# Kernel optimization log

Hardware: AMD Instinct MI355X
Metric: run time of the kernel (lower is better)

## Reference

```python
import jax, jax.numpy as jnp
import numpy as np

MAX_DIST = 32
NUM_HEADS = 16


def setup_inputs() -> dict:
    key = jax.random.key(0)
    ks = jax.random.split(key, 10)
    D = 1024
    B, S = 2, 2048
    hd = D // NUM_HEADS
    sc = 0.02
    return {
        "x": jax.random.normal(ks[0], (B, S, D), dtype=jnp.float32),
        "Wq": jax.random.normal(ks[1], (D, D), dtype=jnp.float32) * sc,
        "bq": jax.random.normal(ks[2], (D,), dtype=jnp.float32) * sc,
        "Wk": jax.random.normal(ks[3], (D, D), dtype=jnp.float32) * sc,
        "bk": jax.random.normal(ks[4], (D,), dtype=jnp.float32) * sc,
        "Wv": jax.random.normal(ks[5], (D, D), dtype=jnp.float32) * sc,
        "bv": jax.random.normal(ks[6], (D,), dtype=jnp.float32) * sc,
        "Wo": jax.random.normal(ks[7], (D, D), dtype=jnp.float32) * sc,
        "bo": jax.random.normal(ks[8], (D,), dtype=jnp.float32) * sc,
        "rel_emb": jax.random.normal(ks[9], (2 * MAX_DIST + 1, hd), dtype=jnp.float32) * sc,
    }


def reference(x, Wq, bq, Wk, bk, Wv, bv, Wo, bo, rel_emb):
    B, S, D = x.shape
    H = NUM_HEADS
    hd = D // H
    scale = hd ** -0.5

    def proj(W, b):
        # [B,S,D] -> [B,H,S,hd]
        return (x @ W + b).reshape(B, S, H, hd).transpose(0, 2, 1, 3)

    q = proj(Wq, bq)
    k = proj(Wk, bk)
    v = proj(Wv, bv)

    # relative position embedding lookup: [S,S,hd]
    pos = jnp.arange(S)
    rel = jnp.clip(pos[:, None] - pos[None, :], -MAX_DIST, MAX_DIST) + MAX_DIST
    rpe = rel_emb[rel]  # [S,S,hd]

    cc = jnp.einsum('bhqd,bhkd->bhqk', q, k) * scale
    cp = jnp.einsum('bhqd,qkd->bhqk', q, rpe) * scale
    attn = jax.nn.softmax(cc + cp, axis=-1)
    ctx = jnp.einsum('bhqk,bhkd->bhqd', attn, v)  # [B,H,S,hd]
    ctx = ctx.transpose(0, 2, 1, 3).reshape(B, S, D)
    return ctx @ Wo + bo
```

## Files before the change

kernel.cpp:

```cpp
#include <hip/hip_runtime.h>

typedef __attribute__((ext_vector_type(4))) float f32x4;
typedef __attribute__((ext_vector_type(8))) short bf16x8;

#define SEQ    2048
#define HD     64
#define NBH    32
#define MTOK   4096
#define DMODEL 1024
#define QBLK   128

__device__ __forceinline__ unsigned short f2b(float f) {
  unsigned int u = __float_as_uint(f);
  u += 0x7fffu + ((u >> 16) & 1u);
  return (unsigned short)(u >> 16);
}
__device__ __forceinline__ float b2f(unsigned short s) {
  return __uint_as_float(((unsigned int)s) << 16);
}
__device__ __forceinline__ unsigned int cvtpk_bf16(float lo, float hi) {
  unsigned int r;
  asm("v_cvt_pk_bf16_f32 %0, %1, %2" : "=v"(r) : "v"(lo), "v"(hi));
  return r;
}
__device__ __forceinline__ void gload16(const void* g, void* l) {
  __builtin_amdgcn_global_load_lds(
      (const __attribute__((address_space(1))) unsigned int*)g,
      (__attribute__((address_space(3))) unsigned int*)l, 16, 0, 0);
}

__global__ __launch_bounds__(256) void k_convert_x(const float* __restrict__ x,
                                                   unsigned short* __restrict__ xb) {
  int i = blockIdx.x * 256 + threadIdx.x;
  float4 v = ((const float4*)x)[i];
  ushort4 o;
  o.x = f2b(v.x); o.y = f2b(v.y); o.z = f2b(v.z); o.w = f2b(v.w);
  ((ushort4*)xb)[i] = o;
}

__global__ __launch_bounds__(256) void k_wtrans_all(const float* __restrict__ Wq,
                                                    const float* __restrict__ Wk,
                                                    const float* __restrict__ Wv,
                                                    const float* __restrict__ Wo,
                                                    unsigned short* __restrict__ Wqkv,
                                                    unsigned short* __restrict__ Wot) {
  __shared__ float tile[64 * 65];
  int z = blockIdx.z;
  const float* W = (z == 0) ? Wq : (z == 1) ? Wk : (z == 2) ? Wv : Wo;
  unsigned short* Wt = (z == 3) ? Wot : Wqkv + (size_t)z * DMODEL * DMODEL;
  int bi = blockIdx.x, bj = blockIdx.y, t = threadIdx.x;
  for (int p = 0; p < 16; p++) {
    int e = p * 256 + t;
    int r = e >> 6, c = e & 63;
    tile[r * 65 + c] = W[(size_t)(bi * 64 + r) * DMODEL + bj * 64 + c];
  }
  __syncthreads();
  for (int p = 0; p < 16; p++) {
    int e = p * 256 + t;
    int n = e >> 6, k = e & 63;
    Wt[(size_t)(bj * 64 + n) * DMODEL + bi * 64 + k] = f2b(tile[k * 65 + n]);
  }
}

template <int MODE>
__global__ __launch_bounds__(256) void k_gemm_bt(
    const unsigned short* __restrict__ A, const unsigned short* __restrict__ Bt,
    int M, int N, int K,
    const float* __restrict__ bias0, const float* __restrict__ bias1,
    const float* __restrict__ bias2,
    float* __restrict__ Cf,
    unsigned short* __restrict__ Qo, unsigned short* __restrict__ Ko,
    unsigned short* __restrict__ Vo) {
  __shared__ unsigned short As[128 * 64];
  __shared__ unsigned short Bs[128 * 64];
  int bm = blockIdx.x, bn = blockIdx.y;
  int tid = threadIdx.x;
  int w = tid >> 6, lane = tid & 63;
  int lg = lane >> 4, lc = lane & 15;
  int wm = (w >> 1) * 64, wn = (w & 1) * 64;
  f32x4 acc[4][4];
  for (int a = 0; a < 4; a++)
    for (int b = 0; b < 4; b++) acc[a][b] = (f32x4){0.f, 0.f, 0.f, 0.f};
  const unsigned short* ag = A + (size_t)(bm * 128) * K;
  const unsigned short* bg = Bt + (size_t)(bn * 128) * K;
  for (int k0 = 0; k0 < K; k0 += 64) {
    __syncthreads();
    for (int p = 0; p < 4; p++) {
      int c = (w * 4 + p) * 64 + lane;
      int r = c >> 3, ch = (c & 7) ^ (r & 7);
      gload16(ag + (size_t)r * K + k0 + ch * 8, &As[c * 8]);
      gload16(bg + (size_t)r * K + k0 + ch * 8, &Bs[c * 8]);
    }
    __syncthreads();
    for (int kk = 0; kk < 2; kk++) {
      bf16x8 av[4], bv[4];
      for (int mi = 0; mi < 4; mi++) {
        int row = wm + mi * 16 + lc;
        av[mi] = *(const bf16x8*)&As[row * 64 + ((kk * 32 + lg * 8) ^ ((row & 7) << 3))];
      }
      for (int ni = 0; ni < 4; ni++) {
        int row = wn + ni * 16 + lc;
        bv[ni] = *(const bf16x8*)&Bs[row * 64 + ((kk * 32 + lg * 8) ^ ((row & 7) << 3))];
      }
      for (int mi = 0; mi < 4; mi++)
        for (int ni = 0; ni < 4; ni++)
          acc[mi][ni] = __builtin_amdgcn_mfma_f32_16x16x32_bf16(av[mi], bv[ni], acc[mi][ni], 0, 0, 0);
    }
  }
  for (int mi = 0; mi < 4; mi++) {
    for (int i = 0; i < 4; i++) {
      int row = bm * 128 + wm + mi * 16 + 4 * lg + i;
      for (int ni = 0; ni < 4; ni++) {
        int col = bn * 128 + wn + ni * 16 + lc;
        float v = acc[mi][ni][i];
        if (MODE == 0) {
          Cf[(size_t)row * N + col] = v + bias0[col];
        } else {
          int which = col >> 10, hcol = col & 1023;
          const float* bb = which == 0 ? bias0 : (which == 1 ? bias1 : bias2);
          unsigned short* dst = which == 0 ? Qo : (which == 1 ? Ko : Vo);
          int b = row >> 11, s = row & 2047;
          int h = hcol >> 6, d = hcol & 63;
          dst[(((size_t)(b * 16 + h)) * SEQ + s) * HD + d] = f2b(v + bb[hcol]);
        }
      }
    }
  }
}

__global__ __launch_bounds__(256) void k_tvqr(const unsigned short* __restrict__ V,
                                              unsigned short* __restrict__ Vt,
                                              const unsigned short* __restrict__ Qb,
                                              const float* __restrict__ rel_emb,
                                              unsigned short* __restrict__ qr) {
  __shared__ unsigned short tile[64 * 72];
  __shared__ float relS[65 * 66];
  __shared__ unsigned short qS[32 * 64];
  int bh = blockIdx.y, t = threadIdx.x;
  if (blockIdx.x < 32) {
    int s0 = blockIdx.x * 64;
    for (int p = 0; p < 16; p++) {
      int e = p * 256 + t;
      int r = e >> 6, c = e & 63;
      tile[r * 72 + c] = V[(((size_t)bh) * SEQ + s0 + r) * HD + c];
    }
    __syncthreads();
    for (int p = 0; p < 16; p++) {
      int e = p * 256 + t;
      int d = e >> 6, j = e & 63;
      Vt[(((size_t)bh) * HD + d) * SEQ + s0 + j] = tile[j * 72 + d];
    }
  } else {
    int s0 = (blockIdx.x - 32) * 32;
    for (int i = t; i < 65 * 64; i += 256) relS[(i >> 6) * 66 + (i & 63)] = rel_emb[i];
    for (int i = t; i < 32 * 64; i += 256) qS[i] = Qb[((size_t)bh * SEQ + s0) * HD + i];
    __syncthreads();
    for (int e = t; e < 32 * 65; e += 256) {
      int sl = e / 65, r = e % 65;
      float acc = 0.f;
      for (int d = 0; d < 64; d++) acc += b2f(qS[sl * 64 + d]) * relS[r * 66 + d];
      qr[((size_t)bh * SEQ + s0 + sl) * 65 + r] = f2b(acc);
    }
  }
}

#define C1 0.180336880f
#define C2 11.5415603f
__global__ __launch_bounds__(512, 4) void k_attn(const unsigned short* __restrict__ Qb,
                                                 const unsigned short* __restrict__ Kb,
                                                 const unsigned short* __restrict__ Vtb,
                                                 const unsigned short* __restrict__ qr,
                                                 unsigned short* __restrict__ ctx) {
  __shared__ unsigned short Ks[64 * 64];
  __shared__ unsigned short Vts[64 * 64];
  __shared__ unsigned short Ps[8][16 * 64];
  __shared__ unsigned short qrs[QBLK * 65];
  int bh = blockIdx.x, qt = blockIdx.y;
  int tid = threadIdx.x, w = tid >> 6, lane = tid & 63;
  int lg = lane >> 4, lc = lane & 15;
  int q0 = qt * QBLK, qw = q0 + w * 16;

  {
    const unsigned int* src = (const unsigned int*)(qr + ((size_t)bh * SEQ + q0) * 65);
    for (int i = tid; i < QBLK * 65 / 2; i += 512) ((unsigned int*)qrs)[i] = src[i];
  }
  bf16x8 aq[2];
  {
    const unsigned short* qp = Qb + ((size_t)bh * SEQ + qw + lc) * HD + lg * 8;
    aq[0] = *(const bf16x8*)qp;
    aq[1] = *(const bf16x8*)(qp + 32);
  }
  f32x4 o[4];
  float l[4];
  for (int n = 0; n < 4; n++) o[n] = (f32x4){0.f, 0.f, 0.f, 0.f};
  for (int i = 0; i < 4; i++) l[i] = 0.f;
  __syncthreads();

  float blo[4], bhi[4];
  for (int i = 0; i < 4; i++) {
    int rl = w * 16 + 4 * lg + i;
    blo[i] = fmaf(b2f(qrs[rl * 65]),      C1, -C2);
    bhi[i] = fmaf(b2f(qrs[rl * 65 + 64]), C1, -C2);
  }

  for (int kt = 0; kt < SEQ / 64; kt++) {
    int k0 = kt * 64;
    const unsigned short* kg = Kb + ((size_t)bh * SEQ + k0) * HD;
    const unsigned short* vg = Vtb + ((size_t)bh * HD) * SEQ + k0;
    {
      int c = tid;
      int r = c >> 3, ch = (c & 7) ^ (r & 7);
      gload16(kg + (size_t)r * HD + ch * 8, &Ks[c * 8]);
      gload16(vg + (size_t)r * SEQ + ch * 8, &Vts[c * 8]);
    }
    __syncthreads();

    f32x4 s[4];
    #pragma unroll
    for (int n = 0; n < 4; n++) s[n] = (f32x4){0.f, 0.f, 0.f, 0.f};
    __builtin_amdgcn_s_setprio(1);
    #pragma unroll
    for (int n = 0; n < 4; n++) {
      int row = n * 16 + lc;
      #pragma unroll
      for (int kk = 0; kk < 2; kk++) {
        bf16x8 bk = *(const bf16x8*)&Ks[row * 64 + ((kk * 32 + lg * 8) ^ ((row & 7) << 3))];
        s[n] = __builtin_amdgcn_mfma_f32_16x16x32_bf16(aq[kk], bk, s[n], 0, 0, 0);
      }
    }
    __builtin_amdgcn_s_setprio(0);

    int dw = qw - k0;
    bool gather = (dw >= -32) && (dw <= 80);
    #pragma unroll
    for (int n = 0; n < 4; n++)
      #pragma unroll
      for (int i = 0; i < 4; i++) {
        float bf;
        if (gather) {
          int rl = w * 16 + 4 * lg + i;
          int rel = rl + q0 - k0 - n * 16 - lc;
          rel = rel < -32 ? -32 : (rel > 32 ? 32 : rel);
          bf = fmaf(b2f(qrs[rl * 65 + rel + 32]), C1, -C2);
        } else {
          bf = (dw < 0) ? blo[i] : bhi[i];
        }
        float p = __builtin_amdgcn_exp2f(fmaf(s[n][i], C1, bf));
        s[n][i] = p;
        l[i] += p;
      }

    #pragma unroll
    for (int n = 0; n < 4; n++)
      #pragma unroll
      for (int i = 0; i < 4; i += 2) {
        unsigned int u = cvtpk_bf16(s[n][i], s[n][i + 1]);
        int r0 = 4 * lg + i, r1 = r0 + 1;
        Ps[w][r0 * 64 + ((n * 16 + lc) ^ ((r0 & 7) << 3))] = (unsigned short)u;
        Ps[w][r1 * 64 + ((n * 16 + lc) ^ ((r1 & 7) << 3))] = (unsigned short)(u >> 16);
      }

    __builtin_amdgcn_s_setprio(1);
    #pragma unroll
    for (int kk = 0; kk < 2; kk++) {
      bf16x8 ap = *(const bf16x8*)&Ps[w][lc * 64 + ((kk * 32 + lg * 8) ^ ((lc & 7) << 3))];
      #pragma unroll
      for (int n = 0; n < 4; n++) {
        int row = n * 16 + lc;
        bf16x8 bv = *(const bf16x8*)&Vts[row * 64 + ((kk * 32 + lg * 8) ^ ((row & 7) << 3))];
        o[n] = __builtin_amdgcn_mfma_f32_16x16x32_bf16(ap, bv, o[n], 0, 0, 0);
      }
    }
    __builtin_amdgcn_s_setprio(0);
    __syncthreads();
  }

  int b = bh >> 4, h = bh & 15;
  for (int i = 0; i < 4; i++) {
    float t = l[i];
    t += __shfl_xor(t, 1);
    t += __shfl_xor(t, 2);
    t += __shfl_xor(t, 4);
    t += __shfl_xor(t, 8);
    float inv = 1.f / t;
    int row = qw + 4 * lg + i;
    size_t base = ((size_t)(b * SEQ + row)) * DMODEL + h * HD;
    for (int n = 0; n < 4; n++) ctx[base + n * 16 + lc] = f2b(o[n][i] * inv);
  }
}

extern "C" void kernel_launch(void* const* d_in, const int* in_sizes, int n_in,
                              void* d_out, int out_size, void* d_ws, size_t ws_size,
                              hipStream_t stream) {
  const float* x   = (const float*)d_in[0];
  const float* Wq  = (const float*)d_in[1];
  const float* bq  = (const float*)d_in[2];
  const float* Wk  = (const float*)d_in[3];
  const float* bk  = (const float*)d_in[4];
  const float* Wv  = (const float*)d_in[5];
  const float* bv  = (const float*)d_in[6];
  const float* Wo  = (const float*)d_in[7];
  const float* bo  = (const float*)d_in[8];
  const float* rel = (const float*)d_in[9];
  float* out = (float*)d_out;

  char* ws = (char*)d_ws;
  size_t off = 0;
  auto carve = [&](size_t bytes) -> void* {
    void* p = ws + off;
    off += (bytes + 255) & ~(size_t)255;
    return p;
  };
  unsigned short* xb   = (unsigned short*)carve((size_t)MTOK * DMODEL * 2);
  unsigned short* Wqkv = (unsigned short*)carve((size_t)3 * DMODEL * DMODEL * 2);
  unsigned short* Wot  = (unsigned short*)carve((size_t)DMODEL * DMODEL * 2);
  unsigned short* Qb   = (unsigned short*)carve((size_t)NBH * SEQ * HD * 2);
  unsigned short* Kb   = (unsigned short*)carve((size_t)NBH * SEQ * HD * 2);
  unsigned short* Vb   = (unsigned short*)carve((size_t)NBH * SEQ * HD * 2);
  unsigned short* Vtb  = (unsigned short*)carve((size_t)NBH * SEQ * HD * 2);
  unsigned short* qr   = (unsigned short*)carve((size_t)NBH * SEQ * 65 * 2);
  unsigned short* ctx  = (unsigned short*)carve((size_t)MTOK * DMODEL * 2);

  k_convert_x<<<MTOK * DMODEL / 4 / 256, 256, 0, stream>>>(x, xb);
  k_wtrans_all<<<dim3(16, 16, 4), 256, 0, stream>>>(Wq, Wk, Wv, Wo, Wqkv, Wot);
  k_gemm_bt<1><<<dim3(32, 24), 256, 0, stream>>>(xb, Wqkv, MTOK, 3 * DMODEL, DMODEL,
                                                 bq, bk, bv, nullptr, Qb, Kb, Vb);
  k_tvqr<<<dim3(96, 32), 256, 0, stream>>>(Vb, Vtb, Qb, rel, qr);
  k_attn<<<dim3(NBH, SEQ / QBLK), 512, 0, stream>>>(Qb, Kb, Vtb, qr, ctx);
  k_gemm_bt<0><<<dim3(32, 8), 256, 0, stream>>>(ctx, Wot, MTOK, DMODEL, DMODEL,
                                                bo, nullptr, nullptr, out,
                                                nullptr, nullptr, nullptr);
}
```

Measured before the change: 174.9 us.

## Give each attention wave 32 query rows to reuse K/V fragments

```diff
diff --git a/kernel.cpp b/kernel.cpp
--- a/kernel.cpp
+++ b/kernel.cpp
@@ -166,58 +166,63 @@
 
 #define C1 0.180336880f
 #define C2 11.5415603f
-__global__ __launch_bounds__(512, 4) void k_attn(const unsigned short* __restrict__ Qb,
+__global__ __launch_bounds__(256, 3) void k_attn(const unsigned short* __restrict__ Qb,
                                                  const unsigned short* __restrict__ Kb,
                                                  const unsigned short* __restrict__ Vtb,
                                                  const unsigned short* __restrict__ qr,
                                                  unsigned short* __restrict__ ctx) {
   __shared__ unsigned short Ks[64 * 64];
   __shared__ unsigned short Vts[64 * 64];
-  __shared__ unsigned short Ps[8][16 * 64];
+  __shared__ unsigned short Ps[4][32 * 64];
   __shared__ unsigned short qrs[QBLK * 65];
   int bh = blockIdx.x, qt = blockIdx.y;
   int tid = threadIdx.x, w = tid >> 6, lane = tid & 63;
   int lg = lane >> 4, lc = lane & 15;
-  int q0 = qt * QBLK, qw = q0 + w * 16;
+  int q0 = qt * QBLK, qw = q0 + w * 32;
 
   {
     const unsigned int* src = (const unsigned int*)(qr + ((size_t)bh * SEQ + q0) * 65);
-    for (int i = tid; i < QBLK * 65 / 2; i += 512) ((unsigned int*)qrs)[i] = src[i];
-  }
-  bf16x8 aq[2];
-  {
-    const unsigned short* qp = Qb + ((size_t)bh * SEQ + qw + lc) * HD + lg * 8;
-    aq[0] = *(const bf16x8*)qp;
-    aq[1] = *(const bf16x8*)(qp + 32);
-  }
-  f32x4 o[4];
-  float l[4];
-  for (int n = 0; n < 4; n++) o[n] = (f32x4){0.f, 0.f, 0.f, 0.f};
-  for (int i = 0; i < 4; i++) l[i] = 0.f;
+    for (int i = tid; i < QBLK * 65 / 2; i += 256) ((unsigned int*)qrs)[i] = src[i];
+  }
+  bf16x8 aq[2][2];
+  for (int m = 0; m < 2; m++) {
+    const unsigned short* qp = Qb + ((size_t)bh * SEQ + qw + m * 16 + lc) * HD + lg * 8;
+    aq[m][0] = *(const bf16x8*)qp;
+    aq[m][1] = *(const bf16x8*)(qp + 32);
+  }
+  f32x4 o[2][4];
+  float l[2][4];
+  for (int m = 0; m < 2; m++)
+    for (int n = 0; n < 4; n++) o[m][n] = (f32x4){0.f, 0.f, 0.f, 0.f};
+  for (int m = 0; m < 2; m++)
+    for (int i = 0; i < 4; i++) l[m][i] = 0.f;
   __syncthreads();
 
-  float blo[4], bhi[4];
-  for (int i = 0; i < 4; i++) {
-    int rl = w * 16 + 4 * lg + i;
-    blo[i] = fmaf(b2f(qrs[rl * 65]),      C1, -C2);
-    bhi[i] = fmaf(b2f(qrs[rl * 65 + 64]), C1, -C2);
-  }
+  float blo[2][4], bhi[2][4];
+  for (int m = 0; m < 2; m++)
+    for (int i = 0; i < 4; i++) {
+      int rl = w * 32 + m * 16 + 4 * lg + i;
+      blo[m][i] = fmaf(b2f(qrs[rl * 65]),      C1, -C2);
+      bhi[m][i] = fmaf(b2f(qrs[rl * 65 + 64]), C1, -C2);
+    }
 
   for (int kt = 0; kt < SEQ / 64; kt++) {
     int k0 = kt * 64;
     const unsigned short* kg = Kb + ((size_t)bh * SEQ + k0) * HD;
     const unsigned short* vg = Vtb + ((size_t)bh * HD) * SEQ + k0;
-    {
-      int c = tid;
-      int r = c >> 3, ch = (c & 7) ^ (r & 7);
-      gload16(kg + (size_t)r * HD + ch * 8, &Ks[c * 8]);
-      gload16(vg + (size_t)r * SEQ + ch * 8, &Vts[c * 8]);
-    }
-    __syncthreads();
-
-    f32x4 s[4];
-    #pragma unroll
-    for (int n = 0; n < 4; n++) s[n] = (f32x4){0.f, 0.f, 0.f, 0.f};
+    #pragma unroll
+    for (int p = 0; p < 2; p++) {
+      int idx = p * 256 + tid;
+      int r = idx >> 3, ch = (idx & 7) ^ (r & 7);
+      gload16(kg + (size_t)r * HD + ch * 8, &Ks[idx * 8]);
+      gload16(vg + (size_t)r * SEQ + ch * 8, &Vts[idx * 8]);
+    }
+    __syncthreads();
+
+    f32x4 s[2][4];
+    #pragma unroll
+    for (int m = 0; m < 2; m++)
+      for (int n = 0; n < 4; n++) s[m][n] = (f32x4){0.f, 0.f, 0.f, 0.f};
     __builtin_amdgcn_s_setprio(1);
     #pragma unroll
     for (int n = 0; n < 4; n++) {
@@ -225,50 +230,59 @@
       #pragma unroll
       for (int kk = 0; kk < 2; kk++) {
         bf16x8 bk = *(const bf16x8*)&Ks[row * 64 + ((kk * 32 + lg * 8) ^ ((row & 7) << 3))];
-        s[n] = __builtin_amdgcn_mfma_f32_16x16x32_bf16(aq[kk], bk, s[n], 0, 0, 0);
+        s[0][n] = __builtin_amdgcn_mfma_f32_16x16x32_bf16(aq[0][kk], bk, s[0][n], 0, 0, 0);
+        s[1][n] = __builtin_amdgcn_mfma_f32_16x16x32_bf16(aq[1][kk], bk, s[1][n], 0, 0, 0);
       }
     }
     __builtin_amdgcn_s_setprio(0);
 
     int dw = qw - k0;
-    bool gather = (dw >= -32) && (dw <= 80);
-    #pragma unroll
-    for (int n = 0; n < 4; n++)
+    bool gather = (dw >= -32) && (dw <= 64);
+    #pragma unroll
+    for (int m = 0; m < 2; m++)
       #pragma unroll
-      for (int i = 0; i < 4; i++) {
-        float bf;
-        if (gather) {
-          int rl = w * 16 + 4 * lg + i;
-          int rel = rl + q0 - k0 - n * 16 - lc;
-          rel = rel < -32 ? -32 : (rel > 32 ? 32 : rel);
-          bf = fmaf(b2f(qrs[rl * 65 + rel + 32]), C1, -C2);
-        } else {
-          bf = (dw < 0) ? blo[i] : bhi[i];
+      for (int n = 0; n < 4; n++)
+        #pragma unroll
+        for (int i = 0; i < 4; i++) {
+          float bf;
+          if (gather) {
+            int rl = w * 32 + m * 16 + 4 * lg + i;
+            int rel = rl + q0 - k0 - n * 16 - lc;
+            rel = rel < -32 ? -32 : (rel > 32 ? 32 : rel);
+            bf = fmaf(b2f(qrs[rl * 65 + rel + 32]), C1, -C2);
+          } else {
+            bf = (dw < 0) ? blo[m][i] : bhi[m][i];
+          }
+          float p = __builtin_amdgcn_exp2f(fmaf(s[m][n][i], C1, bf));
+          s[m][n][i] = p;
+          l[m][i] += p;
         }
-        float p = __builtin_amdgcn_exp2f(fmaf(s[n][i], C1, bf));
-        s[n][i] = p;
-        l[i] += p;
-      }
-
-    #pragma unroll
-    for (int n = 0; n < 4; n++)
+
+    #pragma unroll
+    for (int m = 0; m < 2; m++)
       #pragma unroll
-      for (int i = 0; i < 4; i += 2) {
-        unsigned int u = cvtpk_bf16(s[n][i], s[n][i + 1]);
-        int r0 = 4 * lg + i, r1 = r0 + 1;
-        Ps[w][r0 * 64 + ((n * 16 + lc) ^ ((r0 & 7) << 3))] = (unsigned short)u;
-        Ps[w][r1 * 64 + ((n * 16 + lc) ^ ((r1 & 7) << 3))] = (unsigned short)(u >> 16);
-      }
+      for (int n = 0; n < 4; n++)
+        #pragma unroll
+        for (int i = 0; i < 4; i += 2) {
+          unsigned int u = cvtpk_bf16(s[m][n][i], s[m][n][i + 1]);
+          int r0 = m * 16 + 4 * lg + i;
+          int r1 = r0 + 1;
+          Ps[w][r0 * 64 + ((n * 16 + lc) ^ ((r0 & 7) << 3))] = (unsigned short)u;
+          Ps[w][r1 * 64 + ((n * 16 + lc) ^ ((r1 & 7) << 3))] = (unsigned short)(u >> 16);
+        }
 
     __builtin_amdgcn_s_setprio(1);
     #pragma unroll
     for (int kk = 0; kk < 2; kk++) {
-      bf16x8 ap = *(const bf16x8*)&Ps[w][lc * 64 + ((kk * 32 + lg * 8) ^ ((lc & 7) << 3))];
+      int pr0 = lc, pr1 = 16 + lc;
+      bf16x8 ap0 = *(const bf16x8*)&Ps[w][pr0 * 64 + ((kk * 32 + lg * 8) ^ ((pr0 & 7) << 3))];
+      bf16x8 ap1 = *(const bf16x8*)&Ps[w][pr1 * 64 + ((kk * 32 + lg * 8) ^ ((pr1 & 7) << 3))];
       #pragma unroll
       for (int n = 0; n < 4; n++) {
         int row = n * 16 + lc;
         bf16x8 bv = *(const bf16x8*)&Vts[row * 64 + ((kk * 32 + lg * 8) ^ ((row & 7) << 3))];
-        o[n] = __builtin_amdgcn_mfma_f32_16x16x32_bf16(ap, bv, o[n], 0, 0, 0);
+        o[0][n] = __builtin_amdgcn_mfma_f32_16x16x32_bf16(ap0, bv, o[0][n], 0, 0, 0);
+        o[1][n] = __builtin_amdgcn_mfma_f32_16x16x32_bf16(ap1, bv, o[1][n], 0, 0, 0);
       }
     }
     __builtin_amdgcn_s_setprio(0);
@@ -276,17 +290,18 @@
   }
 
   int b = bh >> 4, h = bh & 15;
-  for (int i = 0; i < 4; i++) {
-    float t = l[i];
-    t += __shfl_xor(t, 1);
-    t += __shfl_xor(t, 2);
-    t += __shfl_xor(t, 4);
-    t += __shfl_xor(t, 8);
-    float inv = 1.f / t;
-    int row = qw + 4 * lg + i;
-    size_t base = ((size_t)(b * SEQ + row)) * DMODEL + h * HD;
-    for (int n = 0; n < 4; n++) ctx[base + n * 16 + lc] = f2b(o[n][i] * inv);
-  }
+  for (int m = 0; m < 2; m++)
+    for (int i = 0; i < 4; i++) {
+      float t = l[m][i];
+      t += __shfl_xor(t, 1);
+      t += __shfl_xor(t, 2);
+      t += __shfl_xor(t, 4);
+      t += __shfl_xor(t, 8);
+      float inv = 1.f / t;
+      int row = qw + m * 16 + 4 * lg + i;
+      size_t base = ((size_t)(b * SEQ + row)) * DMODEL + h * HD;
+      for (int n = 0; n < 4; n++) ctx[base + n * 16 + lc] = f2b(o[m][n][i] * inv);
+    }
 }
 
 extern "C" void kernel_launch(void* const* d_in, const int* in_sizes, int n_in,
@@ -326,7 +341,7 @@
   k_gemm_bt<1><<<dim3(32, 24), 256, 0, stream>>>(xb, Wqkv, MTOK, 3 * DMODEL, DMODEL,
                                                  bq, bk, bv, nullptr, Qb, Kb, Vb);
   k_tvqr<<<dim3(96, 32), 256, 0, stream>>>(Vb, Vtb, Qb, rel, qr);
-  k_attn<<<dim3(NBH, SEQ / QBLK), 512, 0, stream>>>(Qb, Kb, Vtb, qr, ctx);
+  k_attn<<<dim3(NBH, SEQ / QBLK), 256, 0, stream>>>(Qb, Kb, Vtb, qr, ctx);
   k_gemm_bt<0><<<dim3(32, 8), 256, 0, stream>>>(ctx, Wot, MTOK, DMODEL, DMODEL,
                                                 bo, nullptr, nullptr, out,
                                                 nullptr, nullptr, nullptr);
```

Measured after the change: 258.0 us. 47.5% more time.
